# Kernel optimization log

Measured on AMD Instinct MI355X. Metric: run time of the kernel, lower is better.

## Reference

```python
import jax, jax.numpy as jnp
import numpy as np

B, T, D_IN, H, K = 8, 1024, 1024, 1024, 3
PAD = (K - 1) // 2


def conv_gates(x, w, b):
    # x: [B,T,C], w: [3H, C, K], b: [3H] -> f,o,z each [B,T,H]
    y = jax.lax.conv_general_dilated(
        x.transpose(0, 2, 1), w, window_strides=(1,), padding=[(PAD, PAD)],
        dimension_numbers=('NCH', 'OIH', 'NCH'))
    g = y.transpose(0, 2, 1) + b  # [B,T,3H]
    f, o, z = jnp.split(g, 3, axis=-1)
    return jax.nn.sigmoid(f), jax.nn.sigmoid(o), jnp.tanh(z)


def fo_pool(f, z):
    # linear recurrence c_t = f_t*c_{t-1} + (1-f_t)*z_t, c_0 = 0; f,z: [B,T,H]
    def step(c, fz):
        ft, zt = fz
        c = ft * c + (1.0 - ft) * zt
        return c, c
    init = jnp.zeros((f.shape[0], f.shape[2]), f.dtype)
    _, cells = jax.lax.scan(step, init, (f.transpose(1, 0, 2), z.transpose(1, 0, 2)))
    return cells.transpose(1, 0, 2)  # [B,T,H]


def qrnn_layer(x, wf, bf, wr, br):
    # forward direction
    f, o, z = conv_gates(x, wf, bf)
    cells = fo_pool(f, z)
    h = cells * o
    # reverse direction: scan from the end (flip, scan, flip back)
    fr, orv, zr = conv_gates(x, wr, br)
    rcells = jnp.flip(fo_pool(jnp.flip(fr, 1), jnp.flip(zr, 1)), 1)
    rh = rcells * orv
    out = jnp.concatenate([h, rh], -1)                      # [B,T,2H]
    last_h = jnp.concatenate([h[:, -1], rh[:, -1]], -1)     # [B,2H]
    last_c = jnp.concatenate([cells[:, -1], rcells[:, -1]], -1)
    return out, last_h, last_c


def setup_inputs() -> dict:
    key = jax.random.key(0)
    ks = jax.random.split(key, 9)
    x = jax.random.normal(ks[0], (B, T, D_IN), jnp.float32)
    lengths = jnp.full((B,), T, dtype=jnp.int64)
    s = 0.02
    # layer 0: in=D_IN, layer 1: in=2H (bidirectional concat)
    w0f = jax.random.normal(ks[1], (3 * H, D_IN, K), jnp.float32) * s
    b0f = jnp.zeros((3 * H,), jnp.float32)
    w0r = jax.random.normal(ks[2], (3 * H, D_IN, K), jnp.float32) * s
    b0r = jnp.zeros((3 * H,), jnp.float32)
    w1f = jax.random.normal(ks[3], (3 * H, 2 * H, K), jnp.float32) * s
    b1f = jnp.zeros((3 * H,), jnp.float32)
    w1r = jax.random.normal(ks[4], (3 * H, 2 * H, K), jnp.float32) * s
    b1r = jnp.zeros((3 * H,), jnp.float32)
    return {"x": x, "lengths": lengths, "w0f": w0f, "b0f": b0f, "w0r": w0r,
            "b0r": b0r, "w1f": w1f, "b1f": b1f, "w1r": w1r, "b1r": b1r}


def reference(x, lengths, w0f, b0f, w0r, b0r, w1f, b1f, w1r, b1r):
    out0, h0, c0 = qrnn_layer(x, w0f, b0f, w0r, b0r)
    out1, h1, c1 = qrnn_layer(out0, w1f, b1f, w1r, b1r)
    # torch: cat along dim 0 then view(num_dir*num_layers, B, H)
    hidden = jnp.concatenate([h0, h1], 0).reshape(4, x.shape[0], H)
    cell = jnp.concatenate([c0, c1], 0).reshape(4, x.shape[0], H)
    return out1, hidden, cell
```

## Files before the change

### kernel.cpp

```cpp
#include <hip/hip_runtime.h>
#include <math.h>

#define BB 8
#define TT 1024
#define HDIM 1024
#define G3 3072
#define NCH 32
#define TC 32
#define TP (TT + 2)

#define SW(r) (((r) >> 1) & 3)

typedef __attribute__((ext_vector_type(8))) short bf16x8;
typedef __attribute__((ext_vector_type(4))) float f32x4;

__device__ __forceinline__ unsigned short f2bf(float f) {
  union { float f; unsigned int u; } c; c.f = f;
  unsigned int u = c.u;
  return (unsigned short)((u + 0x7FFFu + ((u >> 16) & 1u)) >> 16);
}

__device__ __forceinline__ void load_lds16(const void* g, void* l) {
  __builtin_amdgcn_global_load_lds(
      (const __attribute__((address_space(1))) void*)g,
      (__attribute__((address_space(3))) void*)l, 16, 0, 0);
}

__global__ __launch_bounds__(256) void cvt_x_pad_kernel(const float* __restrict__ in,
                                                        unsigned short* __restrict__ out) {
  int b = blockIdx.y;
  int i = (blockIdx.x * 256 + threadIdx.x) * 4;
  int r = i >> 10;
  int c = i & 1023;
  ushort4 o = make_ushort4(0, 0, 0, 0);
  if (r >= 1 && r <= TT) {
    float4 v = *(const float4*)(in + ((size_t)b * TT + (r - 1)) * 1024 + c);
    o.x = f2bf(v.x); o.y = f2bf(v.y); o.z = f2bf(v.z); o.w = f2bf(v.w);
  }
  *(ushort4*)(out + (size_t)b * TP * 1024 + i) = o;
}

__global__ __launch_bounds__(256) void zero_pad_kernel(unsigned short* __restrict__ p) {
  int i = blockIdx.x * 256 + threadIdx.x;
  int b = i >> 12;
  int r = (i >> 11) & 1;
  int c = i & 2047;
  p[((size_t)b * TP + (r ? (TT + 1) : 0)) * 2048 + c] = 0;
}

template<int C>
__global__ __launch_bounds__(256) void cvt_w_kernel(const float* __restrict__ in,
                                                    unsigned short* __restrict__ out) {
  int o = blockIdx.x * 256 + threadIdx.x;
  int c = o & (C - 1);
  int jk = o / C;
  int j = jk % G3;
  int k = jk / G3;
  out[o] = f2bf(in[(size_t)j * (3 * C) + (size_t)c * 3 + k]);
}

template<int C>
__global__ __launch_bounds__(256, 1) void conv_mfma_kernel(
    const unsigned short* __restrict__ x,
    const unsigned short* __restrict__ wt,
    const float* __restrict__ bias,
    float* __restrict__ g)
{
  const int L    = blockIdx.x;
  const int xcd  = L & 7;
  const int sL   = L >> 3;
  const int jt   = xcd * 2 + (sL & 1);
  const int rest = sL >> 1;
  const int t0 = (rest & 3) * 256;
  const int j0 = jt * 192;
  const int b  = rest >> 2;

  const int tid  = threadIdx.x;
  const int lane = tid & 63;
  const int wave = tid >> 6;
  const int wm = wave >> 1, wn = wave & 1;

  __shared__ unsigned short As[2][272 * 32];
  __shared__ unsigned short Bs[2][576 * 32];

  f32x4 acc[8][6];
  #pragma unroll
  for (int i = 0; i < 8; i++)
    #pragma unroll
    for (int u = 0; u < 6; u++) acc[i][u] = (f32x4){0.f, 0.f, 0.f, 0.f};

  const unsigned short* xb = x + (size_t)b * TP * C;
  const int srow  = lane >> 2;
  const int sslot = lane & 3;
  const int rq = lane >> 4;
  const int rl = lane & 15;

  auto stage = [&](int sel, int c0) {
    unsigned short* Ab = &As[sel][0];
    unsigned short* Bb = &Bs[sel][0];
    #pragma unroll
    for (int cc = 0; cc < 4; ++cc) {
      int lrow0 = (wave * 4 + cc) << 4;
      int lrow  = lrow0 + srow;
      int q = sslot ^ SW(lrow);
      load_lds16(xb + (size_t)(t0 + lrow) * C + c0 + q * 8, Ab + lrow0 * 32);
    }
    if (wave == 3) {
      int lrow0 = 256;
      int lrow  = lrow0 + srow;
      int q = sslot ^ SW(lrow);
      load_lds16(xb + (size_t)(t0 + lrow) * C + c0 + q * 8, Ab + lrow0 * 32);
    }
    #pragma unroll
    for (int cc = 0; cc < 9; ++cc) {
      int R0 = (wave * 9 + cc) << 4;
      int R  = R0 + srow;
      int k  = R / 192;
      int j  = R - k * 192;
      int q  = sslot ^ SW(R);
      load_lds16(wt + (size_t)k * (G3 * C) + (size_t)(j0 + j) * C + c0 + q * 8,
                 Bb + R0 * 32);
    }
  };

  auto ldA = [&](const unsigned short* Ac, bf16x8* d, int k) {
    #pragma unroll
    for (int im = 0; im < 8; ++im) {
      int r = wm * 128 + im * 16 + rl + k;
      d[im] = *(const bf16x8*)&Ac[r * 32 + ((rq ^ SW(r)) * 8)];
    }
  };
  auto ldB = [&](const unsigned short* Bc, bf16x8* d, int k) {
    #pragma unroll
    for (int in = 0; in < 6; ++in) {
      int r = k * 192 + wn * 96 + in * 16 + rl;
      d[in] = *(const bf16x8*)&Bc[r * 32 + ((rq ^ SW(r)) * 8)];
    }
  };
  auto fm = [&](bf16x8* a, bf16x8* bb) {
    #pragma unroll
    for (int im = 0; im < 8; ++im)
      #pragma unroll
      for (int in = 0; in < 6; ++in)
        acc[im][in] = __builtin_amdgcn_mfma_f32_16x16x32_bf16(
            a[im], bb[in], acc[im][in], 0, 0, 0);
  };
  auto compute = [&](int sel) {
    const unsigned short* Ac = &As[sel][0];
    const unsigned short* Bc = &Bs[sel][0];
    bf16x8 a0[8], b0[6], a1[8], b1[6];
    ldA(Ac, a0, 0); ldB(Bc, b0, 0);
    ldA(Ac, a1, 1); ldB(Bc, b1, 1);
    __builtin_amdgcn_s_setprio(1);
    fm(a0, b0);
    ldA(Ac, a0, 2); ldB(Bc, b0, 2);
    fm(a1, b1);
    fm(a0, b0);
    __builtin_amdgcn_s_setprio(0);
  };

  constexpr int NSTEP = C / 32;

  stage(0, 0);

  #pragma unroll 2
  for (int it = 0; it < NSTEP - 1; ++it) {
    const int cur = it & 1;
    stage(cur ^ 1, (it + 1) * 32);
    if (wave == 3) asm volatile("s_waitcnt vmcnt(14)" ::: "memory");
    else           asm volatile("s_waitcnt vmcnt(13)" ::: "memory");
    __builtin_amdgcn_s_barrier();
    __builtin_amdgcn_sched_barrier(0);
    compute(cur);
    __builtin_amdgcn_s_barrier();
  }
  asm volatile("s_waitcnt vmcnt(0)" ::: "memory");
  __builtin_amdgcn_s_barrier();
  __builtin_amdgcn_sched_barrier(0);
  compute((NSTEP - 1) & 1);

  const int row_in_tile = (lane >> 4) * 4;
  float* gb = g + (size_t)b * TT * G3;
  #pragma unroll
  for (int in = 0; in < 6; ++in) {
    int j = j0 + wn * 96 + in * 16 + rl;
    float bv = bias[j];
    const bool is_t = (j >= 2 * HDIM);
    #pragma unroll
    for (int im = 0; im < 8; ++im) {
      int tl = wm * 128 + im * 16 + row_in_tile;
      #pragma unroll
      for (int r = 0; r < 4; ++r) {
        float s = acc[im][in][r] + bv;
        float e = __expf(is_t ? 2.f * s : -s);
        float v = is_t ? (1.f - 2.f / (e + 1.f)) : (1.f / (1.f + e));
        gb[(size_t)(t0 + tl + r) * G3 + j] = v;
      }
    }
  }
}

__global__ __launch_bounds__(256) void pool_chunk_kernel(
    const float* __restrict__ g, float* __restrict__ a_arr,
    float* __restrict__ b_arr, int dir)
{
  int idx = blockIdx.x * 256 + threadIdx.x;
  int h  = idx & (HDIM - 1);
  int b  = (idx >> 10) & (BB - 1);
  int ch = idx >> 13;
  const float* gb = g + (size_t)b * TT * G3 + h;
  float a = 1.f, bacc = 0.f;
  #pragma unroll 8
  for (int s = ch * TC; s < ch * TC + TC; ++s) {
    int t = dir ? (TT - 1 - s) : s;
    size_t go = (size_t)t * G3;
    float f = gb[go];
    float z = gb[go + 2 * HDIM];
    bacc = f * bacc + (1.f - f) * z;
    a *= f;
  }
  a_arr[idx] = a;
  b_arr[idx] = bacc;
}

__global__ __launch_bounds__(256) void pool_scan_kernel(
    const float* __restrict__ a_arr, const float* __restrict__ b_arr,
    float* __restrict__ cinit)
{
  int bh = blockIdx.x * 256 + threadIdx.x;
  float c = 0.f;
  #pragma unroll
  for (int ch = 0; ch < NCH; ++ch) {
    cinit[ch * (BB * HDIM) + bh] = c;
    c = a_arr[ch * (BB * HDIM) + bh] * c + b_arr[ch * (BB * HDIM) + bh];
  }
}

template<int OUT_BF16>
__global__ __launch_bounds__(256) void pool_apply_kernel(
    const float* __restrict__ g, const float* __restrict__ cinit,
    void* __restrict__ out, float* __restrict__ hid, float* __restrict__ cell,
    int dir, int layer)
{
  int idx = blockIdx.x * 256 + threadIdx.x;
  int h  = idx & (HDIM - 1);
  int b  = (idx >> 10) & (BB - 1);
  int ch = idx >> 13;
  const float* gb = g + (size_t)b * TT * G3 + h;
  const int coloff = dir * HDIM;
  float c = cinit[idx];
  #pragma unroll 8
  for (int s = ch * TC; s < ch * TC + TC; ++s) {
    int t = dir ? (TT - 1 - s) : s;
    size_t go = (size_t)t * G3;
    float f = gb[go];
    float o = gb[go + HDIM];
    float z = gb[go + 2 * HDIM];
    c = f * c + (1.f - f) * z;
    float hv = c * o;
    if (OUT_BF16) {
      size_t oo = ((size_t)b * TP + t + 1) * (2 * HDIM) + coloff + h;
      ((unsigned short*)out)[oo] = f2bf(hv);
    } else {
      size_t oo = ((size_t)b * TT + t) * (2 * HDIM) + coloff + h;
      ((float*)out)[oo] = hv;
    }
    if (t == TT - 1) {
      size_t off = (size_t)layer * (BB * 2 * HDIM) + (size_t)b * (2 * HDIM) + coloff + h;
      hid[off] = hv;
      cell[off] = c;
    }
  }
}

extern "C" void kernel_launch(void* const* d_in, const int* in_sizes, int n_in,
                              void* d_out, int out_size, void* d_ws, size_t ws_size,
                              hipStream_t stream) {
  const float* x   = (const float*)d_in[0];
  const float* w0f = (const float*)d_in[2];
  const float* b0f = (const float*)d_in[3];
  const float* w0r = (const float*)d_in[4];
  const float* b0r = (const float*)d_in[5];
  const float* w1f = (const float*)d_in[6];
  const float* b1f = (const float*)d_in[7];
  const float* w1r = (const float*)d_in[8];
  const float* b1r = (const float*)d_in[9];

  float* out1 = (float*)d_out;
  float* hid  = out1 + (size_t)BB * TT * 2 * HDIM;
  float* cell = hid + 4 * BB * HDIM;

  char* ws = (char*)d_ws;
  size_t off = 0;
  float*          g     = (float*)(ws + off);  off += (size_t)BB * TT * G3 * 4;
  unsigned short* out0b = (unsigned short*)(ws + off); off += (size_t)BB * TP * 2 * HDIM * 2;
  unsigned short* xb16  = (unsigned short*)(ws + off); off += (size_t)BB * TP * 1024 * 2;
  unsigned short* wt    = (unsigned short*)(ws + off); off += (size_t)3 * G3 * 2048 * 2;
  float* a_arr = (float*)(ws + off); off += (size_t)NCH * BB * HDIM * 4;
  float* b_arr = (float*)(ws + off); off += (size_t)NCH * BB * HDIM * 4;
  float* cinit = (float*)(ws + off); off += (size_t)NCH * BB * HDIM * 4;

  dim3 blk(256);
  dim3 cgrd(512);
  dim3 chgrd(NCH * BB * HDIM / 256);
  dim3 scgrd(BB * HDIM / 256);

  cvt_x_pad_kernel<<<dim3(TP, BB), blk, 0, stream>>>(x, xb16);
  zero_pad_kernel<<<2 * BB * 2048 / 256, blk, 0, stream>>>(out0b);

  #define RUN_POOL(OUTB, outp, dir, layer)                                         \
    pool_chunk_kernel<<<chgrd, blk, 0, stream>>>(g, a_arr, b_arr, dir);            \
    pool_scan_kernel<<<scgrd, blk, 0, stream>>>(a_arr, b_arr, cinit);              \
    pool_apply_kernel<OUTB><<<chgrd, blk, 0, stream>>>(g, cinit, outp, hid, cell,  \
                                                       dir, layer);

  cvt_w_kernel<1024><<<3 * G3 * 1024 / 256, blk, 0, stream>>>(w0f, wt);
  conv_mfma_kernel<1024><<<cgrd, blk, 0, stream>>>(xb16, wt, b0f, g);
  RUN_POOL(1, out0b, 0, 0)

  cvt_w_kernel<1024><<<3 * G3 * 1024 / 256, blk, 0, stream>>>(w0r, wt);
  conv_mfma_kernel<1024><<<cgrd, blk, 0, stream>>>(xb16, wt, b0r, g);
  RUN_POOL(1, out0b, 1, 0)

  cvt_w_kernel<2048><<<3 * G3 * 2048 / 256, blk, 0, stream>>>(w1f, wt);
  conv_mfma_kernel<2048><<<cgrd, blk, 0, stream>>>(out0b, wt, b1f, g);
  RUN_POOL(0, out1, 0, 1)

  cvt_w_kernel<2048><<<3 * G3 * 2048 / 256, blk, 0, stream>>>(w1r, wt);
  conv_mfma_kernel<2048><<<cgrd, blk, 0, stream>>>(out0b, wt, b1r, g);
  RUN_POOL(0, out1, 1, 1)
  #undef RUN_POOL
}
```

Measured before the change: 1.598 ms.

## Replace double-buffered LDS pipeline with single buffer at two blocks per CU

The conv GEMM kernel drops its double-buffered LDS staging and hand-tuned vmcnt waits. It now uses a single LDS buffer with plain __syncthreads around stage and compute, and raises launch bounds to two blocks per CU. The intent is to hide memory latency through a second resident block instead of through software pipelining inside one block. The risks are register pressure from the large accumulator array under the tighter register limit, and the loss of overlap between loads and MFMA within a block.

```diff
diff --git a/kernel.cpp b/kernel.cpp
--- a/kernel.cpp
+++ b/kernel.cpp
@@ -60,7 +60,7 @@
 }
 
 template<int C>
-__global__ __launch_bounds__(256, 1) void conv_mfma_kernel(
+__global__ __launch_bounds__(256, 2) void conv_mfma_kernel(
     const unsigned short* __restrict__ x,
     const unsigned short* __restrict__ wt,
     const float* __restrict__ bias,
@@ -80,8 +80,8 @@
   const int wave = tid >> 6;
   const int wm = wave >> 1, wn = wave & 1;
 
-  __shared__ unsigned short As[2][272 * 32];
-  __shared__ unsigned short Bs[2][576 * 32];
+  __shared__ unsigned short As[272 * 32];
+  __shared__ unsigned short Bs[576 * 32];
 
   f32x4 acc[8][6];
   #pragma unroll
@@ -95,21 +95,19 @@
   const int rq = lane >> 4;
   const int rl = lane & 15;
 
-  auto stage = [&](int sel, int c0) {
-    unsigned short* Ab = &As[sel][0];
-    unsigned short* Bb = &Bs[sel][0];
+  auto stage = [&](int c0) {
     #pragma unroll
     for (int cc = 0; cc < 4; ++cc) {
       int lrow0 = (wave * 4 + cc) << 4;
       int lrow  = lrow0 + srow;
       int q = sslot ^ SW(lrow);
-      load_lds16(xb + (size_t)(t0 + lrow) * C + c0 + q * 8, Ab + lrow0 * 32);
+      load_lds16(xb + (size_t)(t0 + lrow) * C + c0 + q * 8, &As[lrow0 * 32]);
     }
     if (wave == 3) {
       int lrow0 = 256;
       int lrow  = lrow0 + srow;
       int q = sslot ^ SW(lrow);
-      load_lds16(xb + (size_t)(t0 + lrow) * C + c0 + q * 8, Ab + lrow0 * 32);
+      load_lds16(xb + (size_t)(t0 + lrow) * C + c0 + q * 8, &As[lrow0 * 32]);
     }
     #pragma unroll
     for (int cc = 0; cc < 9; ++cc) {
@@ -119,22 +117,22 @@
       int j  = R - k * 192;
       int q  = sslot ^ SW(R);
       load_lds16(wt + (size_t)k * (G3 * C) + (size_t)(j0 + j) * C + c0 + q * 8,
-                 Bb + R0 * 32);
-    }
-  };
-
-  auto ldA = [&](const unsigned short* Ac, bf16x8* d, int k) {
+                 &Bs[R0 * 32]);
+    }
+  };
+
+  auto ldA = [&](bf16x8* d, int k) {
     #pragma unroll
     for (int im = 0; im < 8; ++im) {
       int r = wm * 128 + im * 16 + rl + k;
-      d[im] = *(const bf16x8*)&Ac[r * 32 + ((rq ^ SW(r)) * 8)];
-    }
-  };
-  auto ldB = [&](const unsigned short* Bc, bf16x8* d, int k) {
+      d[im] = *(const bf16x8*)&As[r * 32 + ((rq ^ SW(r)) * 8)];
+    }
+  };
+  auto ldB = [&](bf16x8* d, int k) {
     #pragma unroll
     for (int in = 0; in < 6; ++in) {
       int r = k * 192 + wn * 96 + in * 16 + rl;
-      d[in] = *(const bf16x8*)&Bc[r * 32 + ((rq ^ SW(r)) * 8)];
+      d[in] = *(const bf16x8*)&Bs[r * 32 + ((rq ^ SW(r)) * 8)];
     }
   };
   auto fm = [&](bf16x8* a, bf16x8* bb) {
@@ -145,39 +143,24 @@
         acc[im][in] = __builtin_amdgcn_mfma_f32_16x16x32_bf16(
             a[im], bb[in], acc[im][in], 0, 0, 0);
   };
-  auto compute = [&](int sel) {
-    const unsigned short* Ac = &As[sel][0];
-    const unsigned short* Bc = &Bs[sel][0];
+  auto compute = [&]() {
     bf16x8 a0[8], b0[6], a1[8], b1[6];
-    ldA(Ac, a0, 0); ldB(Bc, b0, 0);
-    ldA(Ac, a1, 1); ldB(Bc, b1, 1);
+    ldA(a0, 0); ldB(b0, 0);
+    ldA(a1, 1); ldB(b1, 1);
     __builtin_amdgcn_s_setprio(1);
     fm(a0, b0);
-    ldA(Ac, a0, 2); ldB(Bc, b0, 2);
+    ldA(a0, 2); ldB(b0, 2);
     fm(a1, b1);
     fm(a0, b0);
     __builtin_amdgcn_s_setprio(0);
   };
 
-  constexpr int NSTEP = C / 32;
-
-  stage(0, 0);
-
-  #pragma unroll 2
-  for (int it = 0; it < NSTEP - 1; ++it) {
-    const int cur = it & 1;
-    stage(cur ^ 1, (it + 1) * 32);
-    if (wave == 3) asm volatile("s_waitcnt vmcnt(14)" ::: "memory");
-    else           asm volatile("s_waitcnt vmcnt(13)" ::: "memory");
-    __builtin_amdgcn_s_barrier();
-    __builtin_amdgcn_sched_barrier(0);
-    compute(cur);
-    __builtin_amdgcn_s_barrier();
-  }
-  asm volatile("s_waitcnt vmcnt(0)" ::: "memory");
-  __builtin_amdgcn_s_barrier();
-  __builtin_amdgcn_sched_barrier(0);
-  compute((NSTEP - 1) & 1);
+  for (int c0 = 0; c0 < C; c0 += 32) {
+    __syncthreads();
+    stage(c0);
+    __syncthreads();
+    compute();
+  }
 
   const int row_in_tile = (lane >> 4) * 4;
   float* gb = g + (size_t)b * TT * G3;
```

After: 4.944 ms. 3.09x slower.
